# Performance work log

Measured on AMD Instinct MI355X. Metric: run time of the kernel, lower is better.

The kernel has to match this reference:

```python
import jax, jax.numpy as jnp
import numpy as np

N = 4096      # n_nodes
F = 512       # input_dim
R = 64        # repr_dim
H = 8         # n_heads
EPS_BIAS = 0.01
ALPHA = 0.2   # LeakyReLU negative slope
NEG_BIG = 1e16


def setup_inputs() -> dict:
    key = jax.random.key(0)
    k1, k2, k3, k4, k5 = jax.random.split(key, 5)
    node_matrix = jax.random.normal(k1, (N, F), dtype=jnp.float32)
    adjacency_matrix = (jax.random.uniform(k2, (N, N)) < 0.01).astype(jnp.float32)
    adjacency_matrix = jnp.maximum(adjacency_matrix, jnp.eye(N, dtype=jnp.float32))
    # learned parameters (xavier-ish scale)
    W = jax.random.normal(k3, (H, F, R), dtype=jnp.float32) * 0.06
    shared_attention = jax.random.normal(k4, (H, 2 * R), dtype=jnp.float32) * 0.1
    attention_biases = jax.random.normal(k5, (N, N), dtype=jnp.float32) * 0.02
    return {
        "node_matrix": node_matrix,
        "adjacency_matrix": adjacency_matrix,
        "W": W,
        "shared_attention": shared_attention,
        "attention_biases": attention_biases,
    }


def reference(node_matrix, adjacency_matrix, W, shared_attention, attention_biases):
    # hidden_repr: [H, N, R]
    hidden = jnp.einsum('nf,hfr->hnr', node_matrix, W)
    # per-head source/destination scores: [H, N]
    a_src = jnp.einsum('hnr,hr->hn', hidden, shared_attention[:, :R])
    a_dst = jnp.einsum('hnr,hr->hn', hidden, shared_attention[:, R:])
    # broadcast-sum + trainable pair bias: [H, N, N]
    pre = a_src[:, :, None] + a_dst[:, None, :] + EPS_BIAS * attention_biases[None]
    full = jnp.where(pre >= 0, pre, ALPHA * pre)  # LeakyReLU
    # adjacency masking then row softmax
    scores = full + (-NEG_BIG * (1.0 - adjacency_matrix))[None]
    att = jax.nn.softmax(scores, axis=-1)  # [H, N, N]
    # weighted aggregation: [H, N, R]
    out = jnp.einsum('hnm,hmr->hnr', att, hidden)
    # 'concat' aggregation: [N, H*R], head h occupies columns h*R:(h+1)*R
    return jnp.transpose(out, (1, 0, 2)).reshape(N, H * R)
```

## Files before the change

kernel.cpp:

```cpp
#include <hip/hip_runtime.h>
#include <hip/hip_bf16.h>

#define NN 4096
#define FF 512
#define RR 64
#define HH 8
#define HR (HH * RR)
#define CAP 128
#define ATT_STRIDE 132

typedef short bf16x8 __attribute__((ext_vector_type(8)));
typedef float f32x4 __attribute__((ext_vector_type(4)));

__device__ __forceinline__ unsigned short f2bf(float f) {
  __hip_bfloat16 h = __float2bfloat16(f);
  return *reinterpret_cast<unsigned short*>(&h);
}
__device__ __forceinline__ float bf2f(unsigned short u) {
  union { unsigned u32; float f; } cv;
  cv.u32 = ((unsigned)u) << 16;
  return cv.f;
}
__device__ __forceinline__ unsigned nib4(const float4 v) {
  unsigned m = 0;
  if (v.x != 0.f) m |= 1u;
  if (v.y != 0.f) m |= 2u;
  if (v.z != 0.f) m |= 4u;
  if (v.w != 0.f) m |= 8u;
  return m;
}

__global__ __launch_bounds__(256) void k_convert(
    const float* __restrict__ X, const float* __restrict__ W,
    unsigned short* __restrict__ Xb, unsigned short* __restrict__ BbT)
{
  __shared__ unsigned short wt[64][68];
  const int b = blockIdx.x;
  const int tid = threadIdx.x;

  if (b < 2048) {
    const int t = b * 256 + tid;
    const float4 v = reinterpret_cast<const float4*>(X)[t];
    ushort4 u;
    u.x = f2bf(v.x); u.y = f2bf(v.y); u.z = f2bf(v.z); u.w = f2bf(v.w);
    reinterpret_cast<ushort4*>(Xb)[t] = u;
  } else {
    const int b2 = b - 2048;
    const int h = b2 >> 3;
    const int f0 = (b2 & 7) << 6;
    const int fr = tid >> 2;
    const int rq = (tid & 3) << 4;
    const float* wp = W + (size_t)h * FF * RR + (size_t)(f0 + fr) * RR + rq;
#pragma unroll
    for (int v = 0; v < 4; ++v) {
      const float4 x = *reinterpret_cast<const float4*>(wp + v * 4);
      wt[rq + v * 4 + 0][fr] = f2bf(x.x);
      wt[rq + v * 4 + 1][fr] = f2bf(x.y);
      wt[rq + v * 4 + 2][fr] = f2bf(x.z);
      wt[rq + v * 4 + 3][fr] = f2bf(x.w);
    }
    __syncthreads();
    const int r = tid >> 2;
    unsigned short* op = BbT + (size_t)(h * 64 + r) * FF + f0 + ((tid & 3) << 4);
    int4 w0 = *reinterpret_cast<const int4*>(&wt[r][(tid & 3) << 4]);
    int4 w1 = *reinterpret_cast<const int4*>(&wt[r][((tid & 3) << 4) + 8]);
    *reinterpret_cast<int4*>(op) = w0;
    *reinterpret_cast<int4*>(op + 8) = w1;
  }
}

__global__ __launch_bounds__(256) void k_mega(
    const unsigned short* __restrict__ Xb,
    const unsigned short* __restrict__ BbT,
    const float* __restrict__ sa,
    const float* __restrict__ adj,
    const float* __restrict__ bias,
    unsigned short* __restrict__ hiddenT,
    float* __restrict__ a_srcT,
    float* __restrict__ a_dstT,
    int* __restrict__ colsG,
    float* __restrict__ bvalsG,
    int* __restrict__ cnts)
{
  __shared__ unsigned short Als[64 * 32];
  __shared__ unsigned short Bls[64 * 32];
  __shared__ float redS[64][2];
  __shared__ float redD[64][2];
  const int b = blockIdx.x;
  const int tid = threadIdx.x;

  if (b < 512) {
    const int row0 = (b & 63) * 64;
    const int h = b >> 6;
    const int n0 = h * 64;
    const int l = tid & 63;
    const int wid = tid >> 6;
    const int wr = wid >> 1, wc = wid & 1;

    f32x4 acc[2][2];
#pragma unroll
    for (int a = 0; a < 2; ++a)
#pragma unroll
      for (int bb = 0; bb < 2; ++bb) acc[a][bb] = (f32x4){0.f, 0.f, 0.f, 0.f};

    const int srow = tid >> 2;
    const int skel = (tid & 3) * 8;

    for (int k0 = 0; k0 < FF; k0 += 32) {
      const int4 av = *reinterpret_cast<const int4*>(
          &Xb[(size_t)(row0 + srow) * FF + k0 + skel]);
      const int4 bv = *reinterpret_cast<const int4*>(
          &BbT[(size_t)(n0 + srow) * FF + k0 + skel]);
      __syncthreads();
      *reinterpret_cast<int4*>(&Als[tid * 8]) = av;
      *reinterpret_cast<int4*>(&Bls[tid * 8]) = bv;
      __syncthreads();

      const int ka = (l >> 4) * 8;
      const bf16x8 a0 = *reinterpret_cast<const bf16x8*>(&Als[(32 * wr + 0  + (l & 15)) * 32 + ka]);
      const bf16x8 a1 = *reinterpret_cast<const bf16x8*>(&Als[(32 * wr + 16 + (l & 15)) * 32 + ka]);
      const bf16x8 b0 = *reinterpret_cast<const bf16x8*>(&Bls[(32 * wc + 0  + (l & 15)) * 32 + ka]);
      const bf16x8 b1 = *reinterpret_cast<const bf16x8*>(&Bls[(32 * wc + 16 + (l & 15)) * 32 + ka]);
      acc[0][0] = __builtin_amdgcn_mfma_f32_16x16x32_bf16(a0, b0, acc[0][0], 0, 0, 0);
      acc[0][1] = __builtin_amdgcn_mfma_f32_16x16x32_bf16(a0, b1, acc[0][1], 0, 0, 0);
      acc[1][0] = __builtin_amdgcn_mfma_f32_16x16x32_bf16(a1, b0, acc[1][0], 0, 0, 0);
      acc[1][1] = __builtin_amdgcn_mfma_f32_16x16x32_bf16(a1, b1, acc[1][1], 0, 0, 0);
    }

    const int lg = l >> 4;
    const int lc = l & 15;

#pragma unroll
    for (int mi = 0; mi < 2; ++mi)
#pragma unroll
      for (int ni = 0; ni < 2; ++ni)
#pragma unroll
        for (int j = 0; j < 4; ++j) {
          const int rowg = row0 + 32 * wr + 16 * mi + (lg << 2) + j;
          const int colg = n0 + 32 * wc + 16 * ni + lc;
          hiddenT[(size_t)rowg * HR + colg] = f2bf(acc[mi][ni][j]);
        }

    float sS[2], sD[2];
#pragma unroll
    for (int ni = 0; ni < 2; ++ni) {
      const int col = 32 * wc + 16 * ni + lc;
      sS[ni] = sa[(size_t)h * 2 * RR + col];
      sD[ni] = sa[(size_t)h * 2 * RR + RR + col];
    }
#pragma unroll
    for (int mi = 0; mi < 2; ++mi)
#pragma unroll
      for (int j = 0; j < 4; ++j) {
        float ps = acc[mi][0][j] * sS[0] + acc[mi][1][j] * sS[1];
        float pd = acc[mi][0][j] * sD[0] + acc[mi][1][j] * sD[1];
#pragma unroll
        for (int off = 8; off >= 1; off >>= 1) {
          ps += __shfl_xor(ps, off);
          pd += __shfl_xor(pd, off);
        }
        if (lc == 0) {
          const int rl = 32 * wr + 16 * mi + (lg << 2) + j;
          redS[rl][wc] = ps;
          redD[rl][wc] = pd;
        }
      }
    __syncthreads();
    if (tid < 64) {
      a_srcT[(size_t)(row0 + tid) * HH + h] = redS[tid][0] + redS[tid][1];
      a_dstT[(size_t)(row0 + tid) * HH + h] = redD[tid][0] + redD[tid][1];
    }
  } else {
    const int lane = tid & 63;
    const int row = (b - 512) * 4 + (tid >> 6);
    const float* arow = adj + (size_t)row * NN;
    const float* brow = bias + (size_t)row * NN;
    unsigned long long pm = 0;
    {
      float4 buf[8];
#pragma unroll
      for (int c = 0; c < 8; ++c)
        buf[c] = *reinterpret_cast<const float4*>(&arow[c * 256 + (lane << 2)]);
#pragma unroll
      for (int c = 0; c < 8; ++c)
        pm |= (unsigned long long)nib4(buf[c]) << (4 * c);
#pragma unroll
      for (int c = 0; c < 8; ++c)
        buf[c] = *reinterpret_cast<const float4*>(&arow[(c + 8) * 256 + (lane << 2)]);
#pragma unroll
      for (int c = 0; c < 8; ++c)
        pm |= (unsigned long long)nib4(buf[c]) << (4 * c + 32);
    }
    const int cnt = __popcll(pm);
    int pfx = cnt;
#pragma unroll
    for (int off = 1; off < 64; off <<= 1) {
      const int o = __shfl_up(pfx, off);
      if (lane >= off) pfx += o;
    }
    int pos = pfx - cnt;
    unsigned long long m = pm;
    int* cg = colsG + (size_t)row * CAP;
    float* bg = bvalsG + (size_t)row * CAP;
    while (m) {
      const int bit = (int)__builtin_ctzll(m);
      m &= m - 1;
      if (pos < CAP) {
        const int col = ((bit >> 2) << 8) + (lane << 2) + (bit & 3);
        cg[pos] = col;
        bg[pos] = 0.01f * brow[col];
      }
      ++pos;
    }
    const int tot = __shfl(pfx, 63);
    for (int p = tot + lane; p < CAP; p += 64) { cg[p] = 0; bg[p] = 0.f; }
    if (lane == 63) cnts[row] = tot < CAP ? tot : CAP;
  }
}

__global__ __launch_bounds__(128) void k_gat_row(
    const int* __restrict__ colsG,
    const float* __restrict__ bvalsG,
    const int* __restrict__ cnts,
    const float* __restrict__ a_srcT,
    const float* __restrict__ a_dstT,
    const unsigned short* __restrict__ hiddenT,
    float* __restrict__ out)
{
  const int i = blockIdx.x;
  const int tid = threadIdx.x;

  __shared__ __align__(16) float att[HH][ATT_STRIDE];
  __shared__ int cols[CAP];
  __shared__ __align__(16) float accred[2][HR];

  const int c = colsG[(size_t)i * CAP + tid];
  const float b = bvalsG[(size_t)i * CAP + tid];
  const int count = cnts[i];
  const float4 d0 = *reinterpret_cast<const float4*>(&a_dstT[(size_t)c * HH]);
  const float4 d1 = *reinterpret_cast<const float4*>(&a_dstT[(size_t)c * HH + 4]);
  const float4 s0 = *reinterpret_cast<const float4*>(&a_srcT[(size_t)i * HH]);
  const float4 s1 = *reinterpret_cast<const float4*>(&a_srcT[(size_t)i * HH + 4]);

  {
    cols[tid] = c;
    float s;
    s = s0.x + d0.x + b; att[0][tid] = (s >= 0.f) ? s : 0.2f * s;
    s = s0.y + d0.y + b; att[1][tid] = (s >= 0.f) ? s : 0.2f * s;
    s = s0.z + d0.z + b; att[2][tid] = (s >= 0.f) ? s : 0.2f * s;
    s = s0.w + d0.w + b; att[3][tid] = (s >= 0.f) ? s : 0.2f * s;
    s = s1.x + d1.x + b; att[4][tid] = (s >= 0.f) ? s : 0.2f * s;
    s = s1.y + d1.y + b; att[5][tid] = (s >= 0.f) ? s : 0.2f * s;
    s = s1.z + d1.z + b; att[6][tid] = (s >= 0.f) ? s : 0.2f * s;
    s = s1.w + d1.w + b; att[7][tid] = (s >= 0.f) ? s : 0.2f * s;
  }
  __syncthreads();

  {
    const int g = tid >> 4;
    const int l = tid & 15;
    float* arow_h = att[g];
    float m = -3.0e38f;
    for (int t = l; t < count; t += 16) m = fmaxf(m, arow_h[t]);
#pragma unroll
    for (int o = 8; o >= 1; o >>= 1) m = fmaxf(m, __shfl_xor(m, o));
    float ssum = 0.f;
    for (int t = l; t < count; t += 16) {
      const float e = __expf(arow_h[t] - m);
      arow_h[t] = e;
      ssum += e;
    }
#pragma unroll
    for (int o = 8; o >= 1; o >>= 1) ssum += __shfl_xor(ssum, o);
    const float inv = 1.0f / ssum;
    for (int t = l; t < count; t += 16) arow_h[t] *= inv;
  }
  __syncthreads();

  {
    const int g2 = tid >> 6;
    const int o0 = (tid & 63) << 3;
    const float* attrow = att[o0 >> 6];
    const unsigned short* hb = hiddenT + o0;
    const int half = (count + 1) >> 1;
    const int t0 = g2 * half;
    const int t1 = min(t0 + half, count);
    float4 accA = make_float4(0.f, 0.f, 0.f, 0.f);
    float4 accB = make_float4(0.f, 0.f, 0.f, 0.f);
    for (int t = t0; t < t1; ++t) {
      const int cc = cols[t];
      const float a = attrow[t];
      const ushort4 ua = *reinterpret_cast<const ushort4*>(hb + (size_t)cc * HR);
      const ushort4 ub = *reinterpret_cast<const ushort4*>(hb + (size_t)cc * HR + 4);
      accA.x += a * bf2f(ua.x); accA.y += a * bf2f(ua.y);
      accA.z += a * bf2f(ua.z); accA.w += a * bf2f(ua.w);
      accB.x += a * bf2f(ub.x); accB.y += a * bf2f(ub.y);
      accB.z += a * bf2f(ub.z); accB.w += a * bf2f(ub.w);
    }
    *reinterpret_cast<float4*>(&accred[g2][o0]) = accA;
    *reinterpret_cast<float4*>(&accred[g2][o0 + 4]) = accB;
  }
  __syncthreads();
  {
    const int o = tid << 2;
    const float4 v0 = *reinterpret_cast<const float4*>(&accred[0][o]);
    const float4 v1 = *reinterpret_cast<const float4*>(&accred[1][o]);
    const float4 r = make_float4(v0.x + v1.x, v0.y + v1.y, v0.z + v1.z, v0.w + v1.w);
    *reinterpret_cast<float4*>(&out[(size_t)i * HR + o]) = r;
  }
}

extern "C" void kernel_launch(void* const* d_in, const int* in_sizes, int n_in,
                              void* d_out, int out_size, void* d_ws, size_t ws_size,
                              hipStream_t stream) {
  const float* X    = (const float*)d_in[0];
  const float* adj  = (const float*)d_in[1];
  const float* W    = (const float*)d_in[2];
  const float* sa   = (const float*)d_in[3];
  const float* bias = (const float*)d_in[4];
  float* out = (float*)d_out;

  unsigned short* hiddenT = (unsigned short*)d_ws;
  unsigned short* Xb  = hiddenT + (size_t)NN * HR;
  unsigned short* BbT = Xb + (size_t)NN * FF;
  float* a_srcT = (float*)(BbT + (size_t)HR * FF);
  float* a_dstT = a_srcT + (size_t)NN * HH;
  int* cnts     = (int*)(a_dstT + (size_t)NN * HH);
  int* colsG    = cnts + NN;
  float* bvalsG = (float*)(colsG + (size_t)NN * CAP);

  k_convert<<<dim3(2112), 256, 0, stream>>>(X, W, Xb, BbT);
  k_mega<<<dim3(1536), 256, 0, stream>>>(Xb, BbT, sa, adj, bias, hiddenT,
                                         a_srcT, a_dstT, colsG, bvalsG, cnts);
  k_gat_row<<<dim3(NN), 128, 0, stream>>>(colsG, bvalsG, cnts, a_srcT, a_dstT, hiddenT, out);
}
```

Measured before the change: 44.32 us.

## Widen GEMM tile to two heads per block and vectorize hidden gather loads

The projection GEMM part of the fused kernel now computes a 64x128 tile (two heads per block, one head per wave column) instead of 64x64. This halves the number of GEMM blocks and lets each wave reduce a full head's src/dst scores without a shared-memory cross-wave reduction or its extra barrier. In the aggregation kernel, the per-neighbor bf16 row slice is now read with one 16-byte load and unpacked with shifts/masks instead of two 8-byte loads. The trade-off is higher register pressure from more accumulators and fewer GEMM blocks available to overlap with the adjacency-scan blocks.

```diff
diff --git a/kernel.cpp b/kernel.cpp
--- a/kernel.cpp
+++ b/kernel.cpp
@@ -20,6 +20,12 @@
   union { unsigned u32; float f; } cv;
   cv.u32 = ((unsigned)u) << 16;
   return cv.f;
+}
+__device__ __forceinline__ float lo2f(int w) {
+  union { int i; float f; } c; c.i = w << 16; return c.f;
+}
+__device__ __forceinline__ float hi2f(int w) {
+  union { int i; float f; } c; c.i = w & 0xffff0000; return c.f;
 }
 __device__ __forceinline__ unsigned nib4(const float4 v) {
   unsigned m = 0;
@@ -83,25 +89,25 @@
     int* __restrict__ cnts)
 {
   __shared__ unsigned short Als[64 * 32];
-  __shared__ unsigned short Bls[64 * 32];
-  __shared__ float redS[64][2];
-  __shared__ float redD[64][2];
+  __shared__ unsigned short Bls[128 * 32];
   const int b = blockIdx.x;
   const int tid = threadIdx.x;
 
-  if (b < 512) {
-    const int row0 = (b & 63) * 64;
-    const int h = b >> 6;
-    const int n0 = h * 64;
+  if (b < 256) {
+    const int gx = b & 63;
+    const int gy = b >> 6;
+    const int row0 = gx * 64;
+    const int n0 = gy * 128;
     const int l = tid & 63;
     const int wid = tid >> 6;
     const int wr = wid >> 1, wc = wid & 1;
-
-    f32x4 acc[2][2];
+    const int hh = gy * 2 + wc;
+
+    f32x4 acc[2][4];
 #pragma unroll
     for (int a = 0; a < 2; ++a)
 #pragma unroll
-      for (int bb = 0; bb < 2; ++bb) acc[a][bb] = (f32x4){0.f, 0.f, 0.f, 0.f};
+      for (int bb = 0; bb < 4; ++bb) acc[a][bb] = (f32x4){0.f, 0.f, 0.f, 0.f};
 
     const int srow = tid >> 2;
     const int skel = (tid & 3) * 8;
@@ -109,22 +115,31 @@
     for (int k0 = 0; k0 < FF; k0 += 32) {
       const int4 av = *reinterpret_cast<const int4*>(
           &Xb[(size_t)(row0 + srow) * FF + k0 + skel]);
-      const int4 bv = *reinterpret_cast<const int4*>(
+      const int4 bv0 = *reinterpret_cast<const int4*>(
           &BbT[(size_t)(n0 + srow) * FF + k0 + skel]);
+      const int4 bv1 = *reinterpret_cast<const int4*>(
+          &BbT[(size_t)(n0 + 64 + srow) * FF + k0 + skel]);
       __syncthreads();
       *reinterpret_cast<int4*>(&Als[tid * 8]) = av;
-      *reinterpret_cast<int4*>(&Bls[tid * 8]) = bv;
+      *reinterpret_cast<int4*>(&Bls[tid * 8]) = bv0;
+      *reinterpret_cast<int4*>(&Bls[(tid + 256) * 8]) = bv1;
       __syncthreads();
 
       const int ka = (l >> 4) * 8;
       const bf16x8 a0 = *reinterpret_cast<const bf16x8*>(&Als[(32 * wr + 0  + (l & 15)) * 32 + ka]);
       const bf16x8 a1 = *reinterpret_cast<const bf16x8*>(&Als[(32 * wr + 16 + (l & 15)) * 32 + ka]);
-      const bf16x8 b0 = *reinterpret_cast<const bf16x8*>(&Bls[(32 * wc + 0  + (l & 15)) * 32 + ka]);
-      const bf16x8 b1 = *reinterpret_cast<const bf16x8*>(&Bls[(32 * wc + 16 + (l & 15)) * 32 + ka]);
+      const bf16x8 b0 = *reinterpret_cast<const bf16x8*>(&Bls[(64 * wc + 0  + (l & 15)) * 32 + ka]);
+      const bf16x8 b1 = *reinterpret_cast<const bf16x8*>(&Bls[(64 * wc + 16 + (l & 15)) * 32 + ka]);
+      const bf16x8 b2 = *reinterpret_cast<const bf16x8*>(&Bls[(64 * wc + 32 + (l & 15)) * 32 + ka]);
+      const bf16x8 b3 = *reinterpret_cast<const bf16x8*>(&Bls[(64 * wc + 48 + (l & 15)) * 32 + ka]);
       acc[0][0] = __builtin_amdgcn_mfma_f32_16x16x32_bf16(a0, b0, acc[0][0], 0, 0, 0);
       acc[0][1] = __builtin_amdgcn_mfma_f32_16x16x32_bf16(a0, b1, acc[0][1], 0, 0, 0);
+      acc[0][2] = __builtin_amdgcn_mfma_f32_16x16x32_bf16(a0, b2, acc[0][2], 0, 0, 0);
+      acc[0][3] = __builtin_amdgcn_mfma_f32_16x16x32_bf16(a0, b3, acc[0][3], 0, 0, 0);
       acc[1][0] = __builtin_amdgcn_mfma_f32_16x16x32_bf16(a1, b0, acc[1][0], 0, 0, 0);
       acc[1][1] = __builtin_amdgcn_mfma_f32_16x16x32_bf16(a1, b1, acc[1][1], 0, 0, 0);
+      acc[1][2] = __builtin_amdgcn_mfma_f32_16x16x32_bf16(a1, b2, acc[1][2], 0, 0, 0);
+      acc[1][3] = __builtin_amdgcn_mfma_f32_16x16x32_bf16(a1, b3, acc[1][3], 0, 0, 0);
     }
 
     const int lg = l >> 4;
@@ -133,46 +148,43 @@
 #pragma unroll
     for (int mi = 0; mi < 2; ++mi)
 #pragma unroll
-      for (int ni = 0; ni < 2; ++ni)
+      for (int ni = 0; ni < 4; ++ni)
 #pragma unroll
         for (int j = 0; j < 4; ++j) {
           const int rowg = row0 + 32 * wr + 16 * mi + (lg << 2) + j;
-          const int colg = n0 + 32 * wc + 16 * ni + lc;
+          const int colg = n0 + 64 * wc + 16 * ni + lc;
           hiddenT[(size_t)rowg * HR + colg] = f2bf(acc[mi][ni][j]);
         }
 
-    float sS[2], sD[2];
-#pragma unroll
-    for (int ni = 0; ni < 2; ++ni) {
-      const int col = 32 * wc + 16 * ni + lc;
-      sS[ni] = sa[(size_t)h * 2 * RR + col];
-      sD[ni] = sa[(size_t)h * 2 * RR + RR + col];
+    float sS[4], sD[4];
+#pragma unroll
+    for (int ni = 0; ni < 4; ++ni) {
+      const int col = 16 * ni + lc;
+      sS[ni] = sa[(size_t)hh * 2 * RR + col];
+      sD[ni] = sa[(size_t)hh * 2 * RR + RR + col];
     }
 #pragma unroll
     for (int mi = 0; mi < 2; ++mi)
 #pragma unroll
       for (int j = 0; j < 4; ++j) {
-        float ps = acc[mi][0][j] * sS[0] + acc[mi][1][j] * sS[1];
-        float pd = acc[mi][0][j] * sD[0] + acc[mi][1][j] * sD[1];
+        float ps = acc[mi][0][j] * sS[0] + acc[mi][1][j] * sS[1] +
+                   acc[mi][2][j] * sS[2] + acc[mi][3][j] * sS[3];
+        float pd = acc[mi][0][j] * sD[0] + acc[mi][1][j] * sD[1] +
+                   acc[mi][2][j] * sD[2] + acc[mi][3][j] * sD[3];
 #pragma unroll
         for (int off = 8; off >= 1; off >>= 1) {
           ps += __shfl_xor(ps, off);
           pd += __shfl_xor(pd, off);
         }
         if (lc == 0) {
-          const int rl = 32 * wr + 16 * mi + (lg << 2) + j;
-          redS[rl][wc] = ps;
-          redD[rl][wc] = pd;
+          const int rowg = row0 + 32 * wr + 16 * mi + (lg << 2) + j;
+          a_srcT[(size_t)rowg * HH + hh] = ps;
+          a_dstT[(size_t)rowg * HH + hh] = pd;
         }
       }
-    __syncthreads();
-    if (tid < 64) {
-      a_srcT[(size_t)(row0 + tid) * HH + h] = redS[tid][0] + redS[tid][1];
-      a_dstT[(size_t)(row0 + tid) * HH + h] = redD[tid][0] + redD[tid][1];
-    }
   } else {
     const int lane = tid & 63;
-    const int row = (b - 512) * 4 + (tid >> 6);
+    const int row = (b - 256) * 4 + (tid >> 6);
     const float* arow = adj + (size_t)row * NN;
     const float* brow = bias + (size_t)row * NN;
     unsigned long long pm = 0;
@@ -290,12 +302,11 @@
     for (int t = t0; t < t1; ++t) {
       const int cc = cols[t];
       const float a = attrow[t];
-      const ushort4 ua = *reinterpret_cast<const ushort4*>(hb + (size_t)cc * HR);
-      const ushort4 ub = *reinterpret_cast<const ushort4*>(hb + (size_t)cc * HR + 4);
-      accA.x += a * bf2f(ua.x); accA.y += a * bf2f(ua.y);
-      accA.z += a * bf2f(ua.z); accA.w += a * bf2f(ua.w);
-      accB.x += a * bf2f(ub.x); accB.y += a * bf2f(ub.y);
-      accB.z += a * bf2f(ub.z); accB.w += a * bf2f(ub.w);
+      const int4 u = *reinterpret_cast<const int4*>(hb + (size_t)cc * HR);
+      accA.x += a * lo2f(u.x); accA.y += a * hi2f(u.x);
+      accA.z += a * lo2f(u.y); accA.w += a * hi2f(u.y);
+      accB.x += a * lo2f(u.z); accB.y += a * hi2f(u.z);
+      accB.z += a * lo2f(u.w); accB.w += a * hi2f(u.w);
     }
     *reinterpret_cast<float4*>(&accred[g2][o0]) = accA;
     *reinterpret_cast<float4*>(&accred[g2][o0 + 4]) = accB;
@@ -330,7 +341,7 @@
   float* bvalsG = (float*)(colsG + (size_t)NN * CAP);
 
   k_convert<<<dim3(2112), 256, 0, stream>>>(X, W, Xb, BbT);
-  k_mega<<<dim3(1536), 256, 0, stream>>>(Xb, BbT, sa, adj, bias, hiddenT,
+  k_mega<<<dim3(1280), 256, 0, stream>>>(Xb, BbT, sa, adj, bias, hiddenT,
                                          a_srcT, a_dstT, colsG, bvalsG, cnts);
   k_gat_row<<<dim3(NN), 128, 0, stream>>>(colsG, bvalsG, cnts, a_srcT, a_dstT, hiddenT, out);
 }
```

Result: no change. 44.37 us (+0.1%).

## Move adjacency compaction into convert kernel and split GEMM into its own kernel

Applied to the files above, without the earlier changes.

The adjacency scan and compaction now run in the same launch as the X and W bf16 conversion, and the GEMM becomes a standalone 512-block kernel. The memory-bound 64 MB adjacency read can then overlap the conversion traffic instead of sharing a launch with the compute-bound GEMM. The adjacency loads are issued as 16 outstanding float4s per lane instead of two batches of 8, which raises register use. The gather loop also loads 8 bf16 values with one int4 and unpacks them with shift and mask instead of two ushort4 loads.

```diff
diff --git a/kernel.cpp b/kernel.cpp
--- a/kernel.cpp
+++ b/kernel.cpp
@@ -16,10 +16,11 @@
   __hip_bfloat16 h = __float2bfloat16(f);
   return *reinterpret_cast<unsigned short*>(&h);
 }
-__device__ __forceinline__ float bf2f(unsigned short u) {
-  union { unsigned u32; float f; } cv;
-  cv.u32 = ((unsigned)u) << 16;
-  return cv.f;
+__device__ __forceinline__ float lo2f(int w) {
+  union { int i; float f; } c; c.i = w << 16; return c.f;
+}
+__device__ __forceinline__ float hi2f(int w) {
+  union { int i; float f; } c; c.i = w & 0xffff0000; return c.f;
 }
 __device__ __forceinline__ unsigned nib4(const float4 v) {
   unsigned m = 0;
@@ -30,167 +31,32 @@
   return m;
 }
 
-__global__ __launch_bounds__(256) void k_convert(
+__global__ __launch_bounds__(256) void k_stream(
     const float* __restrict__ X, const float* __restrict__ W,
-    unsigned short* __restrict__ Xb, unsigned short* __restrict__ BbT)
+    const float* __restrict__ adj, const float* __restrict__ bias,
+    unsigned short* __restrict__ Xb, unsigned short* __restrict__ BbT,
+    int* __restrict__ colsG, float* __restrict__ bvalsG,
+    int* __restrict__ cnts)
 {
   __shared__ unsigned short wt[64][68];
   const int b = blockIdx.x;
   const int tid = threadIdx.x;
 
-  if (b < 2048) {
-    const int t = b * 256 + tid;
-    const float4 v = reinterpret_cast<const float4*>(X)[t];
-    ushort4 u;
-    u.x = f2bf(v.x); u.y = f2bf(v.y); u.z = f2bf(v.z); u.w = f2bf(v.w);
-    reinterpret_cast<ushort4*>(Xb)[t] = u;
-  } else {
-    const int b2 = b - 2048;
-    const int h = b2 >> 3;
-    const int f0 = (b2 & 7) << 6;
-    const int fr = tid >> 2;
-    const int rq = (tid & 3) << 4;
-    const float* wp = W + (size_t)h * FF * RR + (size_t)(f0 + fr) * RR + rq;
-#pragma unroll
-    for (int v = 0; v < 4; ++v) {
-      const float4 x = *reinterpret_cast<const float4*>(wp + v * 4);
-      wt[rq + v * 4 + 0][fr] = f2bf(x.x);
-      wt[rq + v * 4 + 1][fr] = f2bf(x.y);
-      wt[rq + v * 4 + 2][fr] = f2bf(x.z);
-      wt[rq + v * 4 + 3][fr] = f2bf(x.w);
-    }
-    __syncthreads();
-    const int r = tid >> 2;
-    unsigned short* op = BbT + (size_t)(h * 64 + r) * FF + f0 + ((tid & 3) << 4);
-    int4 w0 = *reinterpret_cast<const int4*>(&wt[r][(tid & 3) << 4]);
-    int4 w1 = *reinterpret_cast<const int4*>(&wt[r][((tid & 3) << 4) + 8]);
-    *reinterpret_cast<int4*>(op) = w0;
-    *reinterpret_cast<int4*>(op + 8) = w1;
-  }
-}
-
-__global__ __launch_bounds__(256) void k_mega(
-    const unsigned short* __restrict__ Xb,
-    const unsigned short* __restrict__ BbT,
-    const float* __restrict__ sa,
-    const float* __restrict__ adj,
-    const float* __restrict__ bias,
-    unsigned short* __restrict__ hiddenT,
-    float* __restrict__ a_srcT,
-    float* __restrict__ a_dstT,
-    int* __restrict__ colsG,
-    float* __restrict__ bvalsG,
-    int* __restrict__ cnts)
-{
-  __shared__ unsigned short Als[64 * 32];
-  __shared__ unsigned short Bls[64 * 32];
-  __shared__ float redS[64][2];
-  __shared__ float redD[64][2];
-  const int b = blockIdx.x;
-  const int tid = threadIdx.x;
-
-  if (b < 512) {
-    const int row0 = (b & 63) * 64;
-    const int h = b >> 6;
-    const int n0 = h * 64;
-    const int l = tid & 63;
-    const int wid = tid >> 6;
-    const int wr = wid >> 1, wc = wid & 1;
-
-    f32x4 acc[2][2];
-#pragma unroll
-    for (int a = 0; a < 2; ++a)
-#pragma unroll
-      for (int bb = 0; bb < 2; ++bb) acc[a][bb] = (f32x4){0.f, 0.f, 0.f, 0.f};
-
-    const int srow = tid >> 2;
-    const int skel = (tid & 3) * 8;
-
-    for (int k0 = 0; k0 < FF; k0 += 32) {
-      const int4 av = *reinterpret_cast<const int4*>(
-          &Xb[(size_t)(row0 + srow) * FF + k0 + skel]);
-      const int4 bv = *reinterpret_cast<const int4*>(
-          &BbT[(size_t)(n0 + srow) * FF + k0 + skel]);
-      __syncthreads();
-      *reinterpret_cast<int4*>(&Als[tid * 8]) = av;
-      *reinterpret_cast<int4*>(&Bls[tid * 8]) = bv;
-      __syncthreads();
-
-      const int ka = (l >> 4) * 8;
-      const bf16x8 a0 = *reinterpret_cast<const bf16x8*>(&Als[(32 * wr + 0  + (l & 15)) * 32 + ka]);
-      const bf16x8 a1 = *reinterpret_cast<const bf16x8*>(&Als[(32 * wr + 16 + (l & 15)) * 32 + ka]);
-      const bf16x8 b0 = *reinterpret_cast<const bf16x8*>(&Bls[(32 * wc + 0  + (l & 15)) * 32 + ka]);
-      const bf16x8 b1 = *reinterpret_cast<const bf16x8*>(&Bls[(32 * wc + 16 + (l & 15)) * 32 + ka]);
-      acc[0][0] = __builtin_amdgcn_mfma_f32_16x16x32_bf16(a0, b0, acc[0][0], 0, 0, 0);
-      acc[0][1] = __builtin_amdgcn_mfma_f32_16x16x32_bf16(a0, b1, acc[0][1], 0, 0, 0);
-      acc[1][0] = __builtin_amdgcn_mfma_f32_16x16x32_bf16(a1, b0, acc[1][0], 0, 0, 0);
-      acc[1][1] = __builtin_amdgcn_mfma_f32_16x16x32_bf16(a1, b1, acc[1][1], 0, 0, 0);
-    }
-
-    const int lg = l >> 4;
-    const int lc = l & 15;
-
-#pragma unroll
-    for (int mi = 0; mi < 2; ++mi)
-#pragma unroll
-      for (int ni = 0; ni < 2; ++ni)
-#pragma unroll
-        for (int j = 0; j < 4; ++j) {
-          const int rowg = row0 + 32 * wr + 16 * mi + (lg << 2) + j;
-          const int colg = n0 + 32 * wc + 16 * ni + lc;
-          hiddenT[(size_t)rowg * HR + colg] = f2bf(acc[mi][ni][j]);
-        }
-
-    float sS[2], sD[2];
-#pragma unroll
-    for (int ni = 0; ni < 2; ++ni) {
-      const int col = 32 * wc + 16 * ni + lc;
-      sS[ni] = sa[(size_t)h * 2 * RR + col];
-      sD[ni] = sa[(size_t)h * 2 * RR + RR + col];
-    }
-#pragma unroll
-    for (int mi = 0; mi < 2; ++mi)
-#pragma unroll
-      for (int j = 0; j < 4; ++j) {
-        float ps = acc[mi][0][j] * sS[0] + acc[mi][1][j] * sS[1];
-        float pd = acc[mi][0][j] * sD[0] + acc[mi][1][j] * sD[1];
-#pragma unroll
-        for (int off = 8; off >= 1; off >>= 1) {
-          ps += __shfl_xor(ps, off);
-          pd += __shfl_xor(pd, off);
-        }
-        if (lc == 0) {
-          const int rl = 32 * wr + 16 * mi + (lg << 2) + j;
-          redS[rl][wc] = ps;
-          redD[rl][wc] = pd;
-        }
-      }
-    __syncthreads();
-    if (tid < 64) {
-      a_srcT[(size_t)(row0 + tid) * HH + h] = redS[tid][0] + redS[tid][1];
-      a_dstT[(size_t)(row0 + tid) * HH + h] = redD[tid][0] + redD[tid][1];
-    }
-  } else {
+  if (b < 1024) {
     const int lane = tid & 63;
-    const int row = (b - 512) * 4 + (tid >> 6);
+    const int row = b * 4 + (tid >> 6);
     const float* arow = adj + (size_t)row * NN;
     const float* brow = bias + (size_t)row * NN;
+
+    float4 buf[16];
+#pragma unroll
+    for (int c = 0; c < 16; ++c)
+      buf[c] = *reinterpret_cast<const float4*>(&arow[c * 256 + (lane << 2)]);
     unsigned long long pm = 0;
-    {
-      float4 buf[8];
-#pragma unroll
-      for (int c = 0; c < 8; ++c)
-        buf[c] = *reinterpret_cast<const float4*>(&arow[c * 256 + (lane << 2)]);
-#pragma unroll
-      for (int c = 0; c < 8; ++c)
-        pm |= (unsigned long long)nib4(buf[c]) << (4 * c);
-#pragma unroll
-      for (int c = 0; c < 8; ++c)
-        buf[c] = *reinterpret_cast<const float4*>(&arow[(c + 8) * 256 + (lane << 2)]);
-#pragma unroll
-      for (int c = 0; c < 8; ++c)
-        pm |= (unsigned long long)nib4(buf[c]) << (4 * c + 32);
-    }
+#pragma unroll
+    for (int c = 0; c < 16; ++c)
+      pm |= (unsigned long long)nib4(buf[c]) << (4 * c);
+
     const int cnt = __popcll(pm);
     int pfx = cnt;
 #pragma unroll
@@ -215,6 +81,131 @@
     const int tot = __shfl(pfx, 63);
     for (int p = tot + lane; p < CAP; p += 64) { cg[p] = 0; bg[p] = 0.f; }
     if (lane == 63) cnts[row] = tot < CAP ? tot : CAP;
+  } else if (b < 3072) {
+    const int t = (b - 1024) * 256 + tid;
+    const float4 v = reinterpret_cast<const float4*>(X)[t];
+    ushort4 u;
+    u.x = f2bf(v.x); u.y = f2bf(v.y); u.z = f2bf(v.z); u.w = f2bf(v.w);
+    reinterpret_cast<ushort4*>(Xb)[t] = u;
+  } else {
+    const int b2 = b - 3072;
+    const int h = b2 >> 3;
+    const int f0 = (b2 & 7) << 6;
+    const int fr = tid >> 2;
+    const int rq = (tid & 3) << 4;
+    const float* wp = W + (size_t)h * FF * RR + (size_t)(f0 + fr) * RR + rq;
+#pragma unroll
+    for (int v = 0; v < 4; ++v) {
+      const float4 x = *reinterpret_cast<const float4*>(wp + v * 4);
+      wt[rq + v * 4 + 0][fr] = f2bf(x.x);
+      wt[rq + v * 4 + 1][fr] = f2bf(x.y);
+      wt[rq + v * 4 + 2][fr] = f2bf(x.z);
+      wt[rq + v * 4 + 3][fr] = f2bf(x.w);
+    }
+    __syncthreads();
+    const int r = tid >> 2;
+    unsigned short* op = BbT + (size_t)(h * 64 + r) * FF + f0 + ((tid & 3) << 4);
+    int4 w0 = *reinterpret_cast<const int4*>(&wt[r][(tid & 3) << 4]);
+    int4 w1 = *reinterpret_cast<const int4*>(&wt[r][((tid & 3) << 4) + 8]);
+    *reinterpret_cast<int4*>(op) = w0;
+    *reinterpret_cast<int4*>(op + 8) = w1;
+  }
+}
+
+__global__ __launch_bounds__(256) void k_gemm(
+    const unsigned short* __restrict__ Xb,
+    const unsigned short* __restrict__ BbT,
+    const float* __restrict__ sa,
+    unsigned short* __restrict__ hiddenT,
+    float* __restrict__ a_srcT,
+    float* __restrict__ a_dstT)
+{
+  __shared__ unsigned short Als[64 * 32];
+  __shared__ unsigned short Bls[64 * 32];
+  __shared__ float redS[64][2];
+  __shared__ float redD[64][2];
+  const int b = blockIdx.x;
+  const int tid = threadIdx.x;
+
+  const int row0 = (b & 63) * 64;
+  const int h = b >> 6;
+  const int n0 = h * 64;
+  const int l = tid & 63;
+  const int wid = tid >> 6;
+  const int wr = wid >> 1, wc = wid & 1;
+
+  f32x4 acc[2][2];
+#pragma unroll
+  for (int a = 0; a < 2; ++a)
+#pragma unroll
+    for (int bb = 0; bb < 2; ++bb) acc[a][bb] = (f32x4){0.f, 0.f, 0.f, 0.f};
+
+  const int srow = tid >> 2;
+  const int skel = (tid & 3) * 8;
+
+  for (int k0 = 0; k0 < FF; k0 += 32) {
+    const int4 av = *reinterpret_cast<const int4*>(
+        &Xb[(size_t)(row0 + srow) * FF + k0 + skel]);
+    const int4 bv = *reinterpret_cast<const int4*>(
+        &BbT[(size_t)(n0 + srow) * FF + k0 + skel]);
+    __syncthreads();
+    *reinterpret_cast<int4*>(&Als[tid * 8]) = av;
+    *reinterpret_cast<int4*>(&Bls[tid * 8]) = bv;
+    __syncthreads();
+
+    const int ka = (l >> 4) * 8;
+    const bf16x8 a0 = *reinterpret_cast<const bf16x8*>(&Als[(32 * wr + 0  + (l & 15)) * 32 + ka]);
+    const bf16x8 a1 = *reinterpret_cast<const bf16x8*>(&Als[(32 * wr + 16 + (l & 15)) * 32 + ka]);
+    const bf16x8 b0 = *reinterpret_cast<const bf16x8*>(&Bls[(32 * wc + 0  + (l & 15)) * 32 + ka]);
+    const bf16x8 b1 = *reinterpret_cast<const bf16x8*>(&Bls[(32 * wc + 16 + (l & 15)) * 32 + ka]);
+    acc[0][0] = __builtin_amdgcn_mfma_f32_16x16x32_bf16(a0, b0, acc[0][0], 0, 0, 0);
+    acc[0][1] = __builtin_amdgcn_mfma_f32_16x16x32_bf16(a0, b1, acc[0][1], 0, 0, 0);
+    acc[1][0] = __builtin_amdgcn_mfma_f32_16x16x32_bf16(a1, b0, acc[1][0], 0, 0, 0);
+    acc[1][1] = __builtin_amdgcn_mfma_f32_16x16x32_bf16(a1, b1, acc[1][1], 0, 0, 0);
+  }
+
+  const int lg = l >> 4;
+  const int lc = l & 15;
+
+#pragma unroll
+  for (int mi = 0; mi < 2; ++mi)
+#pragma unroll
+    for (int ni = 0; ni < 2; ++ni)
+#pragma unroll
+      for (int j = 0; j < 4; ++j) {
+        const int rowg = row0 + 32 * wr + 16 * mi + (lg << 2) + j;
+        const int colg = n0 + 32 * wc + 16 * ni + lc;
+        hiddenT[(size_t)rowg * HR + colg] = f2bf(acc[mi][ni][j]);
+      }
+
+  float sS[2], sD[2];
+#pragma unroll
+  for (int ni = 0; ni < 2; ++ni) {
+    const int col = 32 * wc + 16 * ni + lc;
+    sS[ni] = sa[(size_t)h * 2 * RR + col];
+    sD[ni] = sa[(size_t)h * 2 * RR + RR + col];
+  }
+#pragma unroll
+  for (int mi = 0; mi < 2; ++mi)
+#pragma unroll
+    for (int j = 0; j < 4; ++j) {
+      float ps = acc[mi][0][j] * sS[0] + acc[mi][1][j] * sS[1];
+      float pd = acc[mi][0][j] * sD[0] + acc[mi][1][j] * sD[1];
+#pragma unroll
+      for (int off = 8; off >= 1; off >>= 1) {
+        ps += __shfl_xor(ps, off);
+        pd += __shfl_xor(pd, off);
+      }
+      if (lc == 0) {
+        const int rl = 32 * wr + 16 * mi + (lg << 2) + j;
+        redS[rl][wc] = ps;
+        redD[rl][wc] = pd;
+      }
+    }
+  __syncthreads();
+  if (tid < 64) {
+    a_srcT[(size_t)(row0 + tid) * HH + h] = redS[tid][0] + redS[tid][1];
+    a_dstT[(size_t)(row0 + tid) * HH + h] = redD[tid][0] + redD[tid][1];
   }
 }
 
@@ -290,12 +281,11 @@
     for (int t = t0; t < t1; ++t) {
       const int cc = cols[t];
       const float a = attrow[t];
-      const ushort4 ua = *reinterpret_cast<const ushort4*>(hb + (size_t)cc * HR);
-      const ushort4 ub = *reinterpret_cast<const ushort4*>(hb + (size_t)cc * HR + 4);
-      accA.x += a * bf2f(ua.x); accA.y += a * bf2f(ua.y);
-      accA.z += a * bf2f(ua.z); accA.w += a * bf2f(ua.w);
-      accB.x += a * bf2f(ub.x); accB.y += a * bf2f(ub.y);
-      accB.z += a * bf2f(ub.z); accB.w += a * bf2f(ub.w);
+      const int4 u = *reinterpret_cast<const int4*>(hb + (size_t)cc * HR);
+      accA.x += a * lo2f(u.x); accA.y += a * hi2f(u.x);
+      accA.z += a * lo2f(u.y); accA.w += a * hi2f(u.y);
+      accB.x += a * lo2f(u.z); accB.y += a * hi2f(u.z);
+      accB.z += a * lo2f(u.w); accB.w += a * hi2f(u.w);
     }
     *reinterpret_cast<float4*>(&accred[g2][o0]) = accA;
     *reinterpret_cast<float4*>(&accred[g2][o0 + 4]) = accB;
@@ -329,8 +319,7 @@
   int* colsG    = cnts + NN;
   float* bvalsG = (float*)(colsG + (size_t)NN * CAP);
 
-  k_convert<<<dim3(2112), 256, 0, stream>>>(X, W, Xb, BbT);
-  k_mega<<<dim3(1536), 256, 0, stream>>>(Xb, BbT, sa, adj, bias, hiddenT,
-                                         a_srcT, a_dstT, colsG, bvalsG, cnts);
+  k_stream<<<dim3(3136), 256, 0, stream>>>(X, W, adj, bias, Xb, BbT, colsG, bvalsG, cnts);
+  k_gemm<<<dim3(512), 256, 0, stream>>>(Xb, BbT, sa, hiddenT, a_srcT, a_dstT);
   k_gat_row<<<dim3(NN), 128, 0, stream>>>(colsG, bvalsG, cnts, a_srcT, a_dstT, hiddenT, out);
 }
```

Result: slower. 46.12 us (+4.1%).

## Split fused mega kernel into separate compact and GEMM kernels, gather bias in row kernel

Applied to the files above, without the earlier changes.

Splits the combined GEMM/adjacency-compaction kernel back into two launches, k_compact and k_gemm. The bias gather moves from the compaction stage into the row-attention kernel, which removes the bvalsG workspace write and read round trip. The hidden-row load in the aggregation loop becomes one 16-byte int4 with bit-shift bf16 unpacking instead of two ushort4 loads. In exchange it adds a kernel launch and gives up overlap between the GEMM blocks and the compaction blocks.

```diff
diff --git a/kernel.cpp b/kernel.cpp
--- a/kernel.cpp
+++ b/kernel.cpp
@@ -16,10 +16,11 @@
   __hip_bfloat16 h = __float2bfloat16(f);
   return *reinterpret_cast<unsigned short*>(&h);
 }
-__device__ __forceinline__ float bf2f(unsigned short u) {
-  union { unsigned u32; float f; } cv;
-  cv.u32 = ((unsigned)u) << 16;
-  return cv.f;
+__device__ __forceinline__ float lo2f(int w) {
+  union { int i; float f; } c; c.i = w << 16; return c.f;
+}
+__device__ __forceinline__ float hi2f(int w) {
+  union { int i; float f; } c; c.i = w & 0xffff0000; return c.f;
 }
 __device__ __forceinline__ unsigned nib4(const float4 v) {
   unsigned m = 0;
@@ -69,18 +70,62 @@
   }
 }
 
-__global__ __launch_bounds__(256) void k_mega(
+__global__ __launch_bounds__(256) void k_compact(
+    const float* __restrict__ adj,
+    int* __restrict__ colsG,
+    int* __restrict__ cnts)
+{
+  const int tid = threadIdx.x;
+  const int lane = tid & 63;
+  const int row = blockIdx.x * 4 + (tid >> 6);
+  const float* arow = adj + (size_t)row * NN;
+
+  unsigned long long pm = 0;
+  {
+    float4 buf[8];
+#pragma unroll
+    for (int c = 0; c < 8; ++c)
+      buf[c] = *reinterpret_cast<const float4*>(&arow[c * 256 + (lane << 2)]);
+#pragma unroll
+    for (int c = 0; c < 8; ++c)
+      pm |= (unsigned long long)nib4(buf[c]) << (4 * c);
+#pragma unroll
+    for (int c = 0; c < 8; ++c)
+      buf[c] = *reinterpret_cast<const float4*>(&arow[(c + 8) * 256 + (lane << 2)]);
+#pragma unroll
+    for (int c = 0; c < 8; ++c)
+      pm |= (unsigned long long)nib4(buf[c]) << (4 * c + 32);
+  }
+  const int cnt = __popcll(pm);
+
+  int pfx = cnt;
+#pragma unroll
+  for (int off = 1; off < 64; off <<= 1) {
+    const int o = __shfl_up(pfx, off);
+    if (lane >= off) pfx += o;
+  }
+
+  int pos = pfx - cnt;
+  unsigned long long m = pm;
+  int* cg = colsG + (size_t)row * CAP;
+  while (m) {
+    const int b = (int)__builtin_ctzll(m);
+    m &= m - 1;
+    if (pos < CAP) cg[pos] = ((b >> 2) << 8) + (lane << 2) + (b & 3);
+    ++pos;
+  }
+  const int tot = __shfl(pfx, 63);
+  for (int p = tot + lane; p < CAP; p += 64) cg[p] = 0;
+  if (lane == 63) cnts[row] = tot < CAP ? tot : CAP;
+}
+
+__global__ __launch_bounds__(256) void k_gemm(
     const unsigned short* __restrict__ Xb,
     const unsigned short* __restrict__ BbT,
     const float* __restrict__ sa,
-    const float* __restrict__ adj,
-    const float* __restrict__ bias,
     unsigned short* __restrict__ hiddenT,
     float* __restrict__ a_srcT,
-    float* __restrict__ a_dstT,
-    int* __restrict__ colsG,
-    float* __restrict__ bvalsG,
-    int* __restrict__ cnts)
+    float* __restrict__ a_dstT)
 {
   __shared__ unsigned short Als[64 * 32];
   __shared__ unsigned short Bls[64 * 32];
@@ -89,139 +134,92 @@
   const int b = blockIdx.x;
   const int tid = threadIdx.x;
 
-  if (b < 512) {
-    const int row0 = (b & 63) * 64;
-    const int h = b >> 6;
-    const int n0 = h * 64;
-    const int l = tid & 63;
-    const int wid = tid >> 6;
-    const int wr = wid >> 1, wc = wid & 1;
-
-    f32x4 acc[2][2];
-#pragma unroll
-    for (int a = 0; a < 2; ++a)
-#pragma unroll
-      for (int bb = 0; bb < 2; ++bb) acc[a][bb] = (f32x4){0.f, 0.f, 0.f, 0.f};
-
-    const int srow = tid >> 2;
-    const int skel = (tid & 3) * 8;
-
-    for (int k0 = 0; k0 < FF; k0 += 32) {
-      const int4 av = *reinterpret_cast<const int4*>(
-          &Xb[(size_t)(row0 + srow) * FF + k0 + skel]);
-      const int4 bv = *reinterpret_cast<const int4*>(
-          &BbT[(size_t)(n0 + srow) * FF + k0 + skel]);
-      __syncthreads();
-      *reinterpret_cast<int4*>(&Als[tid * 8]) = av;
-      *reinterpret_cast<int4*>(&Bls[tid * 8]) = bv;
-      __syncthreads();
-
-      const int ka = (l >> 4) * 8;
-      const bf16x8 a0 = *reinterpret_cast<const bf16x8*>(&Als[(32 * wr + 0  + (l & 15)) * 32 + ka]);
-      const bf16x8 a1 = *reinterpret_cast<const bf16x8*>(&Als[(32 * wr + 16 + (l & 15)) * 32 + ka]);
-      const bf16x8 b0 = *reinterpret_cast<const bf16x8*>(&Bls[(32 * wc + 0  + (l & 15)) * 32 + ka]);
-      const bf16x8 b1 = *reinterpret_cast<const bf16x8*>(&Bls[(32 * wc + 16 + (l & 15)) * 32 + ka]);
-      acc[0][0] = __builtin_amdgcn_mfma_f32_16x16x32_bf16(a0, b0, acc[0][0], 0, 0, 0);
-      acc[0][1] = __builtin_amdgcn_mfma_f32_16x16x32_bf16(a0, b1, acc[0][1], 0, 0, 0);
-      acc[1][0] = __builtin_amdgcn_mfma_f32_16x16x32_bf16(a1, b0, acc[1][0], 0, 0, 0);
-      acc[1][1] = __builtin_amdgcn_mfma_f32_16x16x32_bf16(a1, b1, acc[1][1], 0, 0, 0);
+  const int row0 = (b & 63) * 64;
+  const int h = b >> 6;
+  const int n0 = h * 64;
+  const int l = tid & 63;
+  const int wid = tid >> 6;
+  const int wr = wid >> 1, wc = wid & 1;
+
+  f32x4 acc[2][2];
+#pragma unroll
+  for (int a = 0; a < 2; ++a)
+#pragma unroll
+    for (int bb = 0; bb < 2; ++bb) acc[a][bb] = (f32x4){0.f, 0.f, 0.f, 0.f};
+
+  const int srow = tid >> 2;
+  const int skel = (tid & 3) * 8;
+
+  for (int k0 = 0; k0 < FF; k0 += 32) {
+    const int4 av = *reinterpret_cast<const int4*>(
+        &Xb[(size_t)(row0 + srow) * FF + k0 + skel]);
+    const int4 bv = *reinterpret_cast<const int4*>(
+        &BbT[(size_t)(n0 + srow) * FF + k0 + skel]);
+    __syncthreads();
+    *reinterpret_cast<int4*>(&Als[tid * 8]) = av;
+    *reinterpret_cast<int4*>(&Bls[tid * 8]) = bv;
+    __syncthreads();
+
+    const int ka = (l >> 4) * 8;
+    const bf16x8 a0 = *reinterpret_cast<const bf16x8*>(&Als[(32 * wr + 0  + (l & 15)) * 32 + ka]);
+    const bf16x8 a1 = *reinterpret_cast<const bf16x8*>(&Als[(32 * wr + 16 + (l & 15)) * 32 + ka]);
+    const bf16x8 b0 = *reinterpret_cast<const bf16x8*>(&Bls[(32 * wc + 0  + (l & 15)) * 32 + ka]);
+    const bf16x8 b1 = *reinterpret_cast<const bf16x8*>(&Bls[(32 * wc + 16 + (l & 15)) * 32 + ka]);
+    acc[0][0] = __builtin_amdgcn_mfma_f32_16x16x32_bf16(a0, b0, acc[0][0], 0, 0, 0);
+    acc[0][1] = __builtin_amdgcn_mfma_f32_16x16x32_bf16(a0, b1, acc[0][1], 0, 0, 0);
+    acc[1][0] = __builtin_amdgcn_mfma_f32_16x16x32_bf16(a1, b0, acc[1][0], 0, 0, 0);
+    acc[1][1] = __builtin_amdgcn_mfma_f32_16x16x32_bf16(a1, b1, acc[1][1], 0, 0, 0);
+  }
+
+  const int lg = l >> 4;
+  const int lc = l & 15;
+
+#pragma unroll
+  for (int mi = 0; mi < 2; ++mi)
+#pragma unroll
+    for (int ni = 0; ni < 2; ++ni)
+#pragma unroll
+      for (int j = 0; j < 4; ++j) {
+        const int rowg = row0 + 32 * wr + 16 * mi + (lg << 2) + j;
+        const int colg = n0 + 32 * wc + 16 * ni + lc;
+        hiddenT[(size_t)rowg * HR + colg] = f2bf(acc[mi][ni][j]);
+      }
+
+  float sS[2], sD[2];
+#pragma unroll
+  for (int ni = 0; ni < 2; ++ni) {
+    const int col = 32 * wc + 16 * ni + lc;
+    sS[ni] = sa[(size_t)h * 2 * RR + col];
+    sD[ni] = sa[(size_t)h * 2 * RR + RR + col];
+  }
+#pragma unroll
+  for (int mi = 0; mi < 2; ++mi)
+#pragma unroll
+    for (int j = 0; j < 4; ++j) {
+      float ps = acc[mi][0][j] * sS[0] + acc[mi][1][j] * sS[1];
+      float pd = acc[mi][0][j] * sD[0] + acc[mi][1][j] * sD[1];
+#pragma unroll
+      for (int off = 8; off >= 1; off >>= 1) {
+        ps += __shfl_xor(ps, off);
+        pd += __shfl_xor(pd, off);
+      }
+      if (lc == 0) {
+        const int rl = 32 * wr + 16 * mi + (lg << 2) + j;
+        redS[rl][wc] = ps;
+        redD[rl][wc] = pd;
+      }
     }
-
-    const int lg = l >> 4;
-    const int lc = l & 15;
-
-#pragma unroll
-    for (int mi = 0; mi < 2; ++mi)
-#pragma unroll
-      for (int ni = 0; ni < 2; ++ni)
-#pragma unroll
-        for (int j = 0; j < 4; ++j) {
-          const int rowg = row0 + 32 * wr + 16 * mi + (lg << 2) + j;
-          const int colg = n0 + 32 * wc + 16 * ni + lc;
-          hiddenT[(size_t)rowg * HR + colg] = f2bf(acc[mi][ni][j]);
-        }
-
-    float sS[2], sD[2];
-#pragma unroll
-    for (int ni = 0; ni < 2; ++ni) {
-      const int col = 32 * wc + 16 * ni + lc;
-      sS[ni] = sa[(size_t)h * 2 * RR + col];
-      sD[ni] = sa[(size_t)h * 2 * RR + RR + col];
-    }
-#pragma unroll
-    for (int mi = 0; mi < 2; ++mi)
-#pragma unroll
-      for (int j = 0; j < 4; ++j) {
-        float ps = acc[mi][0][j] * sS[0] + acc[mi][1][j] * sS[1];
-        float pd = acc[mi][0][j] * sD[0] + acc[mi][1][j] * sD[1];
-#pragma unroll
-        for (int off = 8; off >= 1; off >>= 1) {
-          ps += __shfl_xor(ps, off);
-          pd += __shfl_xor(pd, off);
-        }
-        if (lc == 0) {
-          const int rl = 32 * wr + 16 * mi + (lg << 2) + j;
-          redS[rl][wc] = ps;
-          redD[rl][wc] = pd;
-        }
-      }
-    __syncthreads();
-    if (tid < 64) {
-      a_srcT[(size_t)(row0 + tid) * HH + h] = redS[tid][0] + redS[tid][1];
-      a_dstT[(size_t)(row0 + tid) * HH + h] = redD[tid][0] + redD[tid][1];
-    }
-  } else {
-    const int lane = tid & 63;
-    const int row = (b - 512) * 4 + (tid >> 6);
-    const float* arow = adj + (size_t)row * NN;
-    const float* brow = bias + (size_t)row * NN;
-    unsigned long long pm = 0;
-    {
-      float4 buf[8];
-#pragma unroll
-      for (int c = 0; c < 8; ++c)
-        buf[c] = *reinterpret_cast<const float4*>(&arow[c * 256 + (lane << 2)]);
-#pragma unroll
-      for (int c = 0; c < 8; ++c)
-        pm |= (unsigned long long)nib4(buf[c]) << (4 * c);
-#pragma unroll
-      for (int c = 0; c < 8; ++c)
-        buf[c] = *reinterpret_cast<const float4*>(&arow[(c + 8) * 256 + (lane << 2)]);
-#pragma unroll
-      for (int c = 0; c < 8; ++c)
-        pm |= (unsigned long long)nib4(buf[c]) << (4 * c + 32);
-    }
-    const int cnt = __popcll(pm);
-    int pfx = cnt;
-#pragma unroll
-    for (int off = 1; off < 64; off <<= 1) {
-      const int o = __shfl_up(pfx, off);
-      if (lane >= off) pfx += o;
-    }
-    int pos = pfx - cnt;
-    unsigned long long m = pm;
-    int* cg = colsG + (size_t)row * CAP;
-    float* bg = bvalsG + (size_t)row * CAP;
-    while (m) {
-      const int bit = (int)__builtin_ctzll(m);
-      m &= m - 1;
-      if (pos < CAP) {
-        const int col = ((bit >> 2) << 8) + (lane << 2) + (bit & 3);
-        cg[pos] = col;
-        bg[pos] = 0.01f * brow[col];
-      }
-      ++pos;
-    }
-    const int tot = __shfl(pfx, 63);
-    for (int p = tot + lane; p < CAP; p += 64) { cg[p] = 0; bg[p] = 0.f; }
-    if (lane == 63) cnts[row] = tot < CAP ? tot : CAP;
+  __syncthreads();
+  if (tid < 64) {
+    a_srcT[(size_t)(row0 + tid) * HH + h] = redS[tid][0] + redS[tid][1];
+    a_dstT[(size_t)(row0 + tid) * HH + h] = redD[tid][0] + redD[tid][1];
   }
 }
 
 __global__ __launch_bounds__(128) void k_gat_row(
     const int* __restrict__ colsG,
-    const float* __restrict__ bvalsG,
     const int* __restrict__ cnts,
+    const float* __restrict__ bias,
     const float* __restrict__ a_srcT,
     const float* __restrict__ a_dstT,
     const unsigned short* __restrict__ hiddenT,
@@ -235,8 +233,8 @@
   __shared__ __align__(16) float accred[2][HR];
 
   const int c = colsG[(size_t)i * CAP + tid];
-  const float b = bvalsG[(size_t)i * CAP + tid];
   const int count = cnts[i];
+  const float b = 0.01f * bias[(size_t)i * NN + c];
   const float4 d0 = *reinterpret_cast<const float4*>(&a_dstT[(size_t)c * HH]);
   const float4 d1 = *reinterpret_cast<const float4*>(&a_dstT[(size_t)c * HH + 4]);
   const float4 s0 = *reinterpret_cast<const float4*>(&a_srcT[(size_t)i * HH]);
@@ -290,12 +288,11 @@
     for (int t = t0; t < t1; ++t) {
       const int cc = cols[t];
       const float a = attrow[t];
-      const ushort4 ua = *reinterpret_cast<const ushort4*>(hb + (size_t)cc * HR);
-      const ushort4 ub = *reinterpret_cast<const ushort4*>(hb + (size_t)cc * HR + 4);
-      accA.x += a * bf2f(ua.x); accA.y += a * bf2f(ua.y);
-      accA.z += a * bf2f(ua.z); accA.w += a * bf2f(ua.w);
-      accB.x += a * bf2f(ub.x); accB.y += a * bf2f(ub.y);
-      accB.z += a * bf2f(ub.z); accB.w += a * bf2f(ub.w);
+      const int4 u = *reinterpret_cast<const int4*>(hb + (size_t)cc * HR);
+      accA.x += a * lo2f(u.x); accA.y += a * hi2f(u.x);
+      accA.z += a * lo2f(u.y); accA.w += a * hi2f(u.y);
+      accB.x += a * lo2f(u.z); accB.y += a * hi2f(u.z);
+      accB.z += a * lo2f(u.w); accB.w += a * hi2f(u.w);
     }
     *reinterpret_cast<float4*>(&accred[g2][o0]) = accA;
     *reinterpret_cast<float4*>(&accred[g2][o0 + 4]) = accB;
@@ -327,10 +324,9 @@
   float* a_dstT = a_srcT + (size_t)NN * HH;
   int* cnts     = (int*)(a_dstT + (size_t)NN * HH);
   int* colsG    = cnts + NN;
-  float* bvalsG = (float*)(colsG + (size_t)NN * CAP);
 
   k_convert<<<dim3(2112), 256, 0, stream>>>(X, W, Xb, BbT);
-  k_mega<<<dim3(1536), 256, 0, stream>>>(Xb, BbT, sa, adj, bias, hiddenT,
-                                         a_srcT, a_dstT, colsG, bvalsG, cnts);
-  k_gat_row<<<dim3(NN), 128, 0, stream>>>(colsG, bvalsG, cnts, a_srcT, a_dstT, hiddenT, out);
-}
+  k_compact<<<dim3(NN / 4), 256, 0, stream>>>(adj, colsG, cnts);
+  k_gemm<<<dim3(512), 256, 0, stream>>>(Xb, BbT, sa, hiddenT, a_srcT, a_dstT);
+  k_gat_row<<<dim3(NN), 128, 0, stream>>>(colsG, cnts, bias, a_srcT, a_dstT, hiddenT, out);
+}
```

After: 48.31 us. 1.09x slower.
